# Optimization experiments

Measured on AMD Instinct MI355X. Metric: run time of the kernel, lower is better.

Reference implementation:

```python
import jax, jax.numpy as jnp
import numpy as np


def setup_inputs() -> dict:
    key = jax.random.key(0)
    k1, k2, k3 = jax.random.split(key, 3)
    B, L, D = 4, 4096, 1024
    inputs = jax.random.normal(k1, (B, L, D), dtype=jnp.float32)
    # nn.Linear(2D, 2D): weight [out=2D, in=2D], bias [2D]
    W_gate = jax.random.normal(k2, (2 * D, 2 * D), dtype=jnp.float32) * (1.0 / np.sqrt(2 * D))
    b_gate = jax.random.normal(k3, (2 * D,), dtype=jnp.float32) * 0.01
    return {"inputs": inputs, "W_gate": W_gate, "b_gate": b_gate}


def reference(inputs, W_gate, b_gate):
    B, L, D = inputs.shape
    # Cumulative average: tril(ones)/arange mask matmul == prefix-mean (linear time)
    denom = jnp.arange(1, L + 1, dtype=inputs.dtype)[None, :, None]  # [1, L, 1]
    average_outputs = jnp.cumsum(inputs, axis=1) / denom  # [B, L, D]
    # Gating linear on concat(inputs, avg): y = x @ W^T + b
    cat = jnp.concatenate([inputs, average_outputs], axis=-1)  # [B, L, 2D]
    gating = jnp.einsum('bld,ed->ble', cat, W_gate) + b_gate  # [B, L, 2D]
    input_gate, forget_gate = jnp.split(gating, 2, axis=-1)
    gating_outputs = (jax.nn.sigmoid(input_gate) * inputs
                      + jax.nn.sigmoid(forget_gate) * average_outputs)
    return gating_outputs, average_outputs
```

## Files before the change

kernel.cpp:

```cpp
#include <hip/hip_runtime.h>

#define B_   4
#define L_   4096
#define D_   1024
#define ROWS (B_ * L_)
#define K2   (2 * D_)
#define BLD  (ROWS * D_)
#define CH   64
#define NC   64

typedef __attribute__((ext_vector_type(8))) short s8v;
typedef __attribute__((ext_vector_type(4))) float f4v;

__device__ __forceinline__ unsigned short f2bf(float f) {
    unsigned int u = __float_as_uint(f);
    u += 0x7FFFu + ((u >> 16) & 1u);
    return (unsigned short)(u >> 16);
}
__device__ __forceinline__ float sigmoidf_(float v) {
    return 1.0f / (1.0f + __expf(-v));
}
__device__ __forceinline__ void llds16(const void* g, void* l) {
    __builtin_amdgcn_global_load_lds(
        (const __attribute__((address_space(1))) unsigned int*)(g),
        (__attribute__((address_space(3))) unsigned int*)(l),
        16, 0, 0);
}
#define MEMFENCE asm volatile("" ::: "memory")
#define SBAR do { MEMFENCE; __builtin_amdgcn_s_barrier(); MEMFENCE; } while (0)


__global__ void prep1(const float4* __restrict__ x4, float4* __restrict__ part4,
                      const float4* __restrict__ W, ushort4* __restrict__ Wbf) {
    int bid = blockIdx.x;
    int t = threadIdx.x;
    if (bid < 256) {
        int c = bid & 63, b = bid >> 6;
        const float4* p = x4 + ((size_t)(b * L_ + c * CH) * 256 + t);
        float4 s; s.x = 0.f; s.y = 0.f; s.z = 0.f; s.w = 0.f;
#pragma unroll 8
        for (int i = 0; i < CH; ++i) {
            float4 v = p[(size_t)i * 256];
            s.x += v.x; s.y += v.y; s.z += v.z; s.w += v.w;
        }
        part4[(size_t)bid * 256 + t] = s;
    } else {
        int i = (bid - 256) * 256 + t;
        float4 v = W[i];
        ushort4 o; o.x = f2bf(v.x); o.y = f2bf(v.y); o.z = f2bf(v.z); o.w = f2bf(v.w);
        Wbf[i] = o;
    }
}

__global__ void apply_scan(const float4* __restrict__ x4, const float4* __restrict__ part4,
                           float4* __restrict__ avg4, ushort4* __restrict__ A4) {
    __shared__ float inv[CH];
    int bid = blockIdx.x;
    int c = bid & 63, b = bid >> 6;
    int t = threadIdx.x;
    if (t < CH) inv[t] = 1.0f / (float)(c * CH + t + 1);

    float4 s; s.x = 0.f; s.y = 0.f; s.z = 0.f; s.w = 0.f;
    for (int cc = 0; cc < c; ++cc) {
        float4 v = part4[((size_t)(b * NC + cc)) * 256 + t];
        s.x += v.x; s.y += v.y; s.z += v.z; s.w += v.w;
    }
    __syncthreads();

    size_t row0 = (size_t)b * L_ + (size_t)c * CH;
    const float4* px = x4 + (row0 * 256 + t);
    float4*       pa = avg4 + (row0 * 256 + t);
    ushort4*      pA = A4 + (row0 * 512 + t);
#pragma unroll 4
    for (int i = 0; i < CH; ++i) {
        float4 v = px[(size_t)i * 256];
        s.x += v.x; s.y += v.y; s.z += v.z; s.w += v.w;
        float r = inv[i];
        float4 av; av.x = s.x * r; av.y = s.y * r; av.z = s.z * r; av.w = s.w * r;
        pa[(size_t)i * 256] = av;
        ushort4 ux; ux.x = f2bf(v.x);  ux.y = f2bf(v.y);  ux.z = f2bf(v.z);  ux.w = f2bf(v.w);
        ushort4 ua; ua.x = f2bf(av.x); ua.y = f2bf(av.y); ua.z = f2bf(av.z); ua.w = f2bf(av.w);
        pA[(size_t)i * 512]       = ux;
        pA[(size_t)i * 512 + 256] = ua;
    }
}

__global__ __launch_bounds__(512, 2) void gemm_gated8(
        const unsigned short* __restrict__ Abf, const unsigned short* __restrict__ Wbf,
        const float* __restrict__ x, const float* __restrict__ avg,
        const float* __restrict__ bg, float* __restrict__ out) {
    __shared__ __attribute__((aligned(16))) unsigned short S[4 * 2 * 8192];

    const int t    = threadIdx.x;
    const int w    = t >> 6;
    const int lane = t & 63;
    const int wm = w >> 1, wn = w & 1;
    const int quad = lane >> 4, lcol = lane & 15;

    const int bid = blockIdx.x;
    const int swz = (bid & 7) * 64 + (bid >> 3);
    const int tileN = swz & 7, tileM = swz >> 3;
    const int row0 = tileM * 256, col0 = tileN * 128;

    f4v acc0[4][4], acc1[4][4];
#pragma unroll
    for (int i = 0; i < 4; ++i)
#pragma unroll
        for (int j = 0; j < 4; ++j)
#pragma unroll
            for (int r = 0; r < 4; ++r) { acc0[i][j][r] = 0.f; acc1[i][j][r] = 0.f; }

    const int qA0 = t, qA1 = 512 + t;
    const int p0 = qA0 ^ ((qA0 >> 2) & 3);
    const int p1 = qA1 ^ ((qA1 >> 2) & 3);
    const int m0 = p0 >> 2, k0e = (p0 & 3) * 8;
    const int m1 = p1 >> 2, k1e = (p1 & 3) * 8;
    const unsigned short* gA0 = Abf + (size_t)(row0 + m0) * K2 + k0e;
    const unsigned short* gA1 = Abf + (size_t)(row0 + m1) * K2 + k1e;
    const unsigned short* gB0 = Wbf + (size_t)(col0 + (m0 & 127) + (m0 >> 7) * 1024) * K2 + k0e;
    const unsigned short* gB1 = Wbf + (size_t)(col0 + (m1 & 127) + (m1 >> 7) * 1024) * K2 + k1e;

    int aoff[4], boff[2][4];
#pragma unroll
    for (int i = 0; i < 4; ++i)
        aoff[i] = ((((wm * 64 + i * 16 + lcol) * 64) + quad * 16) ^ ((lcol & 3) << 4)) >> 1;
#pragma unroll
    for (int h = 0; h < 2; ++h)
#pragma unroll
        for (int j = 0; j < 4; ++j)
            boff[h][j] = ((((h * 128 + wn * 64 + j * 16 + lcol) * 64) + quad * 16) ^ ((lcol & 3) << 4)) >> 1;

#pragma unroll
    for (int tt = 0; tt < 3; ++tt) {
        unsigned short* dA = S + tt * 16384;
        unsigned short* dB = S + tt * 16384 + 8192;
        llds16(gA0 + tt * 32, dA + qA0 * 8);
        llds16(gA1 + tt * 32, dA + qA1 * 8);
        llds16(gB0 + tt * 32, dB + qA0 * 8);
        llds16(gB1 + tt * 32, dB + qA1 * 8);
    }
    asm volatile("s_waitcnt vmcnt(8)" ::: "memory");
    SBAR;

#pragma unroll 4
    for (int tau = 0; tau < 64; ++tau) {
        const unsigned short* bA = S + (tau & 3) * 16384;
        const unsigned short* bB = bA + 8192;
        const int st = tau + 3;
        unsigned short* dA = S + (st & 3) * 16384;
        unsigned short* dB = dA + 8192;
        const bool do_stage = st < 64;
        const int ko = st * 32;

        s8v af[4], bf[4];
#pragma unroll
        for (int i = 0; i < 4; ++i) af[i] = *(const s8v*)(bA + aoff[i]);
#pragma unroll
        for (int j = 0; j < 4; ++j) bf[j] = *(const s8v*)(bB + boff[0][j]);
        if (do_stage) {
            llds16(gA0 + ko, dA + qA0 * 8);
            llds16(gA1 + ko, dA + qA1 * 8);
        }
        SBAR;
        __builtin_amdgcn_s_setprio(1);
#pragma unroll
        for (int i = 0; i < 4; ++i)
#pragma unroll
            for (int j = 0; j < 4; ++j)
                acc0[i][j] = __builtin_amdgcn_mfma_f32_16x16x32_bf16(af[i], bf[j], acc0[i][j], 0, 0, 0);
        __builtin_amdgcn_s_setprio(0);
        SBAR;

#pragma unroll
        for (int j = 0; j < 4; ++j) bf[j] = *(const s8v*)(bB + boff[1][j]);
        if (do_stage) {
            llds16(gB0 + ko, dB + qA0 * 8);
            llds16(gB1 + ko, dB + qA1 * 8);
        }
        asm volatile("s_waitcnt vmcnt(8)" ::: "memory");
        SBAR;
        __builtin_amdgcn_s_setprio(1);
#pragma unroll
        for (int i = 0; i < 4; ++i)
#pragma unroll
            for (int j = 0; j < 4; ++j)
                acc1[i][j] = __builtin_amdgcn_mfma_f32_16x16x32_bf16(af[i], bf[j], acc1[i][j], 0, 0, 0);
        __builtin_amdgcn_s_setprio(0);
        SBAR;
    }

    float b1v[4], b2v[4];
#pragma unroll
    for (int j = 0; j < 4; ++j) {
        int cc = col0 + wn * 64 + j * 16 + lcol;
        b1v[j] = bg[cc];
        b2v[j] = bg[1024 + cc];
    }
#pragma unroll
    for (int i = 0; i < 4; ++i) {
#pragma unroll
        for (int j = 0; j < 4; ++j) {
            int rr = row0 + wm * 64 + i * 16 + quad * 4;
            int cc = col0 + wn * 64 + j * 16 + lcol;
#pragma unroll
            for (int r = 0; r < 4; ++r) {
                size_t off = (size_t)(rr + r) * D_ + cc;
                float gi = sigmoidf_(acc0[i][j][r] + b1v[j]);
                float gf = sigmoidf_(acc1[i][j][r] + b2v[j]);
                out[off] = gi * x[off] + gf * avg[off];
            }
        }
    }
}

extern "C" void kernel_launch(void* const* d_in, const int* in_sizes, int n_in,
                              void* d_out, int out_size, void* d_ws, size_t ws_size,
                              hipStream_t stream) {
    const float* x  = (const float*)d_in[0];
    const float* W  = (const float*)d_in[1];
    const float* bg = (const float*)d_in[2];
    float* out = (float*)d_out;
    float* avg = out + (size_t)BLD;

    char* ws = (char*)d_ws;
    unsigned short* Abf = (unsigned short*)(ws);
    unsigned short* Wbf = (unsigned short*)(ws + (size_t)67108864);
    float4*         prt = (float4*)(ws + (size_t)75497472);

    prep1<<<dim3(4352), dim3(256), 0, stream>>>((const float4*)x, prt,
                                                (const float4*)W, (ushort4*)Wbf);
    apply_scan<<<dim3(256), dim3(256), 0, stream>>>((const float4*)x, prt,
                                                    (float4*)avg, (ushort4*)Abf);
    gemm_gated8<<<dim3(512), dim3(512), 0, stream>>>(Abf, Wbf, x, avg, bg, out);
}
```

Baseline: 365.7 us.

## Restructure GEMM main loop with register double-buffered fragments and fewer barriers

Rewrites the bf16 MFMA main loop so A and first-half B fragments for the next k-step are prefetched into a second register set while the current MFMAs run. All four global-to-LDS loads are issued together once per iteration, and barriers drop from four per step to two, with sched_barrier and explicit lgkmcnt/vmcnt waits. The LDS layout and XOR swizzle are simplified. Fragment offsets become constant strides, and the loop is manually unrolled with explicit tail handling. The aim is to hide LDS latency and cut synchronization cost, at the price of more registers and fragile hand-tuned wait counts.

```diff
diff --git a/kernel.cpp b/kernel.cpp
--- a/kernel.cpp
+++ b/kernel.cpp
@@ -26,8 +26,6 @@
         (__attribute__((address_space(3))) unsigned int*)(l),
         16, 0, 0);
 }
-#define MEMFENCE asm volatile("" ::: "memory")
-#define SBAR do { MEMFENCE; __builtin_amdgcn_s_barrier(); MEMFENCE; } while (0)
 
 
 __global__ void prep1(const float4* __restrict__ x4, float4* __restrict__ part4,
@@ -85,11 +83,67 @@
     }
 }
 
+#define TAU_ITER(CUR, NXT, TAU, DO_STAGE, DO_PF, VMSTR)                        \
+  {                                                                            \
+    const int tau_ = (TAU);                                                    \
+    const unsigned short* bB_ = S + (tau_ & 3) * 16384 + 8192;                 \
+    s8v b1f[4];                                                                \
+    _Pragma("unroll")                                                          \
+    for (int j = 0; j < 4; ++j)                                                \
+      b1f[j] = *(const s8v*)(bB_ + boffb + 4096 + j * 512);                    \
+    __builtin_amdgcn_sched_barrier(0);                                         \
+    if (DO_STAGE) {                                                            \
+      const int ko_ = (tau_ + 3) * 32;                                         \
+      unsigned short* dA_ = S + ((tau_ + 3) & 3) * 16384;                      \
+      llds16(gA0 + ko_, dA_ + qA0 * 8);                                        \
+      llds16(gA0 + 262144 + ko_, dA_ + qA1 * 8);                               \
+      llds16(gB0 + ko_, dA_ + 8192 + qA0 * 8);                                 \
+      llds16(gB0 + 2097152 + ko_, dA_ + 8192 + qA1 * 8);                       \
+    }                                                                          \
+    asm volatile("s_waitcnt vmcnt(" VMSTR ")" ::: "memory");                   \
+    __builtin_amdgcn_s_barrier();                                              \
+    asm volatile("s_waitcnt lgkmcnt(4)");                                      \
+    __builtin_amdgcn_sched_barrier(0);                                         \
+    __builtin_amdgcn_s_setprio(1);                                             \
+    _Pragma("unroll")                                                          \
+    for (int i = 0; i < 4; ++i)                                                \
+      _Pragma("unroll")                                                        \
+      for (int j = 0; j < 4; ++j)                                              \
+        acc0[i][j] = __builtin_amdgcn_mfma_f32_16x16x32_bf16(                  \
+            afr[CUR][i], bf0r[CUR][j], acc0[i][j], 0, 0, 0);                   \
+    __builtin_amdgcn_s_setprio(0);                                             \
+    __builtin_amdgcn_sched_barrier(0);                                         \
+    if (DO_PF) {                                                               \
+      const unsigned short* bA_n = S + ((tau_ + 1) & 3) * 16384;               \
+      _Pragma("unroll")                                                        \
+      for (int i = 0; i < 4; ++i)                                              \
+        afr[NXT][i] = *(const s8v*)(bA_n + aoff0 + i * 512);                   \
+      _Pragma("unroll")                                                        \
+      for (int j = 0; j < 4; ++j)                                              \
+        bf0r[NXT][j] = *(const s8v*)(bA_n + 8192 + boffb + j * 512);           \
+      __builtin_amdgcn_sched_barrier(0);                                       \
+      asm volatile("s_waitcnt lgkmcnt(8)");                                    \
+    } else {                                                                   \
+      asm volatile("s_waitcnt lgkmcnt(0)");                                    \
+    }                                                                          \
+    __builtin_amdgcn_sched_barrier(0);                                         \
+    __builtin_amdgcn_s_setprio(1);                                             \
+    _Pragma("unroll")                                                          \
+    for (int i = 0; i < 4; ++i)                                                \
+      _Pragma("unroll")                                                        \
+      for (int j = 0; j < 4; ++j)                                              \
+        acc1[i][j] = __builtin_amdgcn_mfma_f32_16x16x32_bf16(                  \
+            afr[CUR][i], b1f[j], acc1[i][j], 0, 0, 0);                         \
+    __builtin_amdgcn_s_setprio(0);                                             \
+    __builtin_amdgcn_sched_barrier(0);                                         \
+    __builtin_amdgcn_s_barrier();                                              \
+  }
+
 __global__ __launch_bounds__(512, 2) void gemm_gated8(
         const unsigned short* __restrict__ Abf, const unsigned short* __restrict__ Wbf,
         const float* __restrict__ x, const float* __restrict__ avg,
         const float* __restrict__ bg, float* __restrict__ out) {
-    __shared__ __attribute__((aligned(16))) unsigned short S[4 * 2 * 8192];
+    __shared__ __attribute__((aligned(16))) unsigned short S[4 * 16384];
 
     const int t    = threadIdx.x;
     const int w    = t >> 6;
@@ -111,83 +165,42 @@
             for (int r = 0; r < 4; ++r) { acc0[i][j][r] = 0.f; acc1[i][j][r] = 0.f; }
 
     const int qA0 = t, qA1 = 512 + t;
-    const int p0 = qA0 ^ ((qA0 >> 2) & 3);
-    const int p1 = qA1 ^ ((qA1 >> 2) & 3);
+    const int p0 = qA0 ^ ((qA0 >> 3) & 3);
     const int m0 = p0 >> 2, k0e = (p0 & 3) * 8;
-    const int m1 = p1 >> 2, k1e = (p1 & 3) * 8;
     const unsigned short* gA0 = Abf + (size_t)(row0 + m0) * K2 + k0e;
-    const unsigned short* gA1 = Abf + (size_t)(row0 + m1) * K2 + k1e;
-    const unsigned short* gB0 = Wbf + (size_t)(col0 + (m0 & 127) + (m0 >> 7) * 1024) * K2 + k0e;
-    const unsigned short* gB1 = Wbf + (size_t)(col0 + (m1 & 127) + (m1 >> 7) * 1024) * K2 + k1e;
-
-    int aoff[4], boff[2][4];
-#pragma unroll
-    for (int i = 0; i < 4; ++i)
-        aoff[i] = ((((wm * 64 + i * 16 + lcol) * 64) + quad * 16) ^ ((lcol & 3) << 4)) >> 1;
-#pragma unroll
-    for (int h = 0; h < 2; ++h)
-#pragma unroll
-        for (int j = 0; j < 4; ++j)
-            boff[h][j] = ((((h * 128 + wn * 64 + j * 16 + lcol) * 64) + quad * 16) ^ ((lcol & 3) << 4)) >> 1;
+    const unsigned short* gB0 = Wbf + (size_t)(col0 + m0) * K2 + k0e;
+
+    const int swzx  = ((lcol >> 1) & 3) << 3;
+    const int aoff0 = ((wm * 64 + lcol) * 32 + quad * 8) ^ swzx;
+    const int boffb = ((wn * 64 + lcol) * 32 + quad * 8) ^ swzx;
 
 #pragma unroll
     for (int tt = 0; tt < 3; ++tt) {
         unsigned short* dA = S + tt * 16384;
-        unsigned short* dB = S + tt * 16384 + 8192;
-        llds16(gA0 + tt * 32, dA + qA0 * 8);
-        llds16(gA1 + tt * 32, dA + qA1 * 8);
-        llds16(gB0 + tt * 32, dB + qA0 * 8);
-        llds16(gB1 + tt * 32, dB + qA1 * 8);
+        const int ko = tt * 32;
+        llds16(gA0 + ko, dA + qA0 * 8);
+        llds16(gA0 + 262144 + ko, dA + qA1 * 8);
+        llds16(gB0 + ko, dA + 8192 + qA0 * 8);
+        llds16(gB0 + 2097152 + ko, dA + 8192 + qA1 * 8);
     }
     asm volatile("s_waitcnt vmcnt(8)" ::: "memory");
-    SBAR;
-
-#pragma unroll 4
-    for (int tau = 0; tau < 64; ++tau) {
-        const unsigned short* bA = S + (tau & 3) * 16384;
-        const unsigned short* bB = bA + 8192;
-        const int st = tau + 3;
-        unsigned short* dA = S + (st & 3) * 16384;
-        unsigned short* dB = dA + 8192;
-        const bool do_stage = st < 64;
-        const int ko = st * 32;
-
-        s8v af[4], bf[4];
-#pragma unroll
-        for (int i = 0; i < 4; ++i) af[i] = *(const s8v*)(bA + aoff[i]);
-#pragma unroll
-        for (int j = 0; j < 4; ++j) bf[j] = *(const s8v*)(bB + boff[0][j]);
-        if (do_stage) {
-            llds16(gA0 + ko, dA + qA0 * 8);
-            llds16(gA1 + ko, dA + qA1 * 8);
-        }
-        SBAR;
-        __builtin_amdgcn_s_setprio(1);
-#pragma unroll
-        for (int i = 0; i < 4; ++i)
-#pragma unroll
-            for (int j = 0; j < 4; ++j)
-                acc0[i][j] = __builtin_amdgcn_mfma_f32_16x16x32_bf16(af[i], bf[j], acc0[i][j], 0, 0, 0);
-        __builtin_amdgcn_s_setprio(0);
-        SBAR;
-
-#pragma unroll
-        for (int j = 0; j < 4; ++j) bf[j] = *(const s8v*)(bB + boff[1][j]);
-        if (do_stage) {
-            llds16(gB0 + ko, dB + qA0 * 8);
-            llds16(gB1 + ko, dB + qA1 * 8);
-        }
-        asm volatile("s_waitcnt vmcnt(8)" ::: "memory");
-        SBAR;
-        __builtin_amdgcn_s_setprio(1);
-#pragma unroll
-        for (int i = 0; i < 4; ++i)
-#pragma unroll
-            for (int j = 0; j < 4; ++j)
-                acc1[i][j] = __builtin_amdgcn_mfma_f32_16x16x32_bf16(af[i], bf[j], acc1[i][j], 0, 0, 0);
-        __builtin_amdgcn_s_setprio(0);
-        SBAR;
-    }
+    __builtin_amdgcn_s_barrier();
+
+    s8v afr[2][4], bf0r[2][4];
+#pragma unroll
+    for (int i = 0; i < 4; ++i) afr[0][i] = *(const s8v*)(S + aoff0 + i * 512);
+#pragma unroll
+    for (int j = 0; j < 4; ++j) bf0r[0][j] = *(const s8v*)(S + 8192 + boffb + j * 512);
+    __builtin_amdgcn_sched_barrier(0);
+
+    for (int tp = 0; tp < 30; ++tp) {
+        TAU_ITER(0, 1, 2 * tp,     true, true, "8");
+        TAU_ITER(1, 0, 2 * tp + 1, true, true, "8");
+    }
+    TAU_ITER(0, 1, 60, true,  true,  "8");
+    TAU_ITER(1, 0, 61, false, true,  "4");
+    TAU_ITER(0, 1, 62, false, true,  "0");
+    TAU_ITER(1, 0, 63, false, false, "0");
 
     float b1v[4], b2v[4];
 #pragma unroll
```

Result: faster. 352.6 us (-3.6%).
